# Optimization experiments

Measured on AMD Instinct MI355X. Metric: run time of the kernel, lower is better.

## Reference

```python
import jax, jax.numpy as jnp
import numpy as np
import math

B, S, D, H = 4, 512, 128, 4
HD = D // H
NEG = float(-2**32 + 1)

def _ln(x, g, b, eps=1e-8):
    m = jnp.mean(x, axis=-1, keepdims=True)
    v = jnp.var(x, axis=-1, keepdims=True)
    return (x - m) * jax.lax.rsqrt(v + eps) * g + b

def setup_inputs() -> dict:
    key = jax.random.key(0)
    ks = jax.random.split(key, 16)
    s = 0.02
    inp = {
        'embed': jax.random.normal(ks[0], (B, S, D), jnp.float32),
        'time_matrix_K': jax.random.normal(ks[1], (B, S, S, D), jnp.float32),
        'time_matrix_V': jax.random.normal(ks[2], (B, S, S, D), jnp.float32),
        # causal additive mask: large negative above diagonal (1--mask semantics)
        'attn_mask': jnp.where(jnp.triu(jnp.ones((S, S), bool), k=1), jnp.float32(-1e9), jnp.float32(0.0)),
        'padding_mask': jnp.zeros((B, S), bool),
        'wq': jax.random.normal(ks[3], (D, D), jnp.float32) * s,
        'bq': jnp.zeros((D,), jnp.float32),
        'wk': jax.random.normal(ks[4], (D, D), jnp.float32) * s,
        'bk': jnp.zeros((D,), jnp.float32),
        'wv': jax.random.normal(ks[5], (D, D), jnp.float32) * s,
        'bv': jnp.zeros((D,), jnp.float32),
        'wo': jax.random.normal(ks[6], (D, D), jnp.float32) * s,
        'bo': jnp.zeros((D,), jnp.float32),
        'ln1_g': jnp.ones((D,), jnp.float32),
        'ln1_b': jnp.zeros((D,), jnp.float32),
        'ln2_g': jnp.ones((D,), jnp.float32),
        'ln2_b': jnp.zeros((D,), jnp.float32),
        'w1': jax.random.normal(ks[7], (D, D), jnp.float32) * s,  # d_ff defaults to d_model
        'b1': jnp.zeros((D,), jnp.float32),
        'w2': jax.random.normal(ks[8], (D, D), jnp.float32) * s,
        'b2': jnp.zeros((D,), jnp.float32),
    }
    return inp

def reference(embed, time_matrix_K, time_matrix_V, attn_mask, padding_mask,
              wq, bq, wk, bk, wv, bv, wo, bo,
              ln1_g, ln1_b, ln2_g, ln2_b, w1, b1, w2, b2):
    # Pre-LN on Q only (K, V take raw embed), per original block
    Qn = _ln(embed, ln1_g, ln1_b)
    q = (Qn @ wq + bq).reshape(B, S, H, HD).transpose(0, 2, 1, 3)      # bhqd
    k = (embed @ wk + bk).reshape(B, S, H, HD).transpose(0, 2, 1, 3)   # bhkd
    v = (embed @ wv + bv).reshape(B, S, H, HD).transpose(0, 2, 1, 3)   # bhkd
    tmK = time_matrix_K.reshape(B, S, S, H, HD).transpose(0, 3, 1, 2, 4)  # bhqkd
    tmV = time_matrix_V.reshape(B, S, S, H, HD).transpose(0, 3, 1, 2, 4)  # bhqkd
    scale = math.sqrt(HD)
    energy = jnp.einsum('bhqd,bhkd->bhqk', q, k)
    energy = energy + jnp.einsum('bhqkd,bhqd->bhqk', tmK, q)
    energy = energy / scale
    energy = energy + attn_mask[None, None]
    energy = jnp.where(padding_mask[:, None, None, :], jnp.float32(NEG), energy)
    attn = jax.nn.softmax(energy, axis=-1)  # dropout is identity in eval
    O = jnp.einsum('bhqk,bhkd->bhqd', attn, v)
    O = O + jnp.einsum('bhqk,bhqkd->bhqd', attn, tmV)
    O = O.transpose(0, 2, 1, 3).reshape(B, S, D)
    O = O @ wo + bo
    x = Qn + O                      # residual adds LN'd Q, per original code
    x = _ln(x, ln2_g, ln2_b)
    ff = jax.nn.gelu(x @ w1 + b1, approximate=False) @ w2 + b2
    return ff + x
```

## Files before the change

kernel.cpp:

```cpp
#include <hip/hip_runtime.h>
#include <math.h>

#define Bsz 4
#define Ssz 512
#define Dsz 128
#define Hsz 4
#define HDsz 32
#define KT 64
#define NT 8

typedef float floatx4 __attribute__((ext_vector_type(4)));

static __device__ __forceinline__ float4 ldnt4(const float* p) {
    floatx4 v = __builtin_nontemporal_load(reinterpret_cast<const floatx4*>(p));
    float4 r; r.x = v.x; r.y = v.y; r.z = v.z; r.w = v.w;
    return r;
}

__global__ __launch_bounds__(128) void k_pre(
    const float* __restrict__ embed,
    const float* __restrict__ wq, const float* __restrict__ bq,
    const float* __restrict__ wk, const float* __restrict__ bk,
    const float* __restrict__ wv, const float* __restrict__ bv,
    const float* __restrict__ g1, const float* __restrict__ b1,
    float* __restrict__ Qn, float* __restrict__ Qs,
    float* __restrict__ Kp, float* __restrict__ Vp)
{
    __shared__ float xs[4][128];
    __shared__ float qs[4][128];
    const int t = threadIdx.x;
    const int row0 = blockIdx.x * 4;
    const int r = t >> 5;
    const int c = t & 31;
    const int d4 = c << 2;

    const float4* e4 = (const float4*)(embed + (size_t)row0 * Dsz);
    float4 x4 = e4[r * 32 + c];

    float s = x4.x + x4.y + x4.z + x4.w;
    #pragma unroll
    for (int o = 1; o < 32; o <<= 1) s += __shfl_xor(s, o);
    const float m = s * (1.0f / 128.0f);

    const float dx0 = x4.x - m, dx1 = x4.y - m, dx2 = x4.z - m, dx3 = x4.w - m;
    float vs = dx0*dx0 + dx1*dx1 + dx2*dx2 + dx3*dx3;
    #pragma unroll
    for (int o = 1; o < 32; o <<= 1) vs += __shfl_xor(vs, o);
    const float rstd = rsqrtf(vs * (1.0f / 128.0f) + 1e-8f);

    const float4 g4 = *(const float4*)(g1 + d4);
    const float4 bb4 = *(const float4*)(b1 + d4);
    float4 qn4;
    qn4.x = dx0 * rstd * g4.x + bb4.x;
    qn4.y = dx1 * rstd * g4.y + bb4.y;
    qn4.z = dx2 * rstd * g4.z + bb4.z;
    qn4.w = dx3 * rstd * g4.w + bb4.w;

    xs[r][d4+0] = x4.x; xs[r][d4+1] = x4.y; xs[r][d4+2] = x4.z; xs[r][d4+3] = x4.w;
    qs[r][d4+0] = qn4.x; qs[r][d4+1] = qn4.y; qs[r][d4+2] = qn4.z; qs[r][d4+3] = qn4.w;
    *(float4*)(Qn + (size_t)(row0 + r) * Dsz + d4) = qn4;
    __syncthreads();

    float aq[4] = {0,0,0,0}, ak[4] = {0,0,0,0}, av[4] = {0,0,0,0};
    for (int d = 0; d < 128; ++d) {
        const float wqv = wq[d*128 + t];
        const float wkv = wk[d*128 + t];
        const float wvv = wv[d*128 + t];
        #pragma unroll
        for (int rr = 0; rr < 4; ++rr) {
            aq[rr] += qs[rr][d] * wqv;
            ak[rr] += xs[rr][d] * wkv;
            av[rr] += xs[rr][d] * wvv;
        }
    }
    const float inv_scale = 0.17677669529663687f;
    const float bqv = bq[t], bkv = bk[t], bvv = bv[t];
    #pragma unroll
    for (int rr = 0; rr < 4; ++rr) {
        const size_t o = (size_t)(row0 + rr) * Dsz + t;
        Qs[o] = (aq[rr] + bqv) * inv_scale;
        Kp[o] = ak[rr] + bkv;
        Vp[o] = av[rr] + bvv;
    }
}

__global__ __launch_bounds__(256) void k_attn_tile(
    const float* __restrict__ tmK, const float* __restrict__ tmV,
    const float* __restrict__ Qs, const float* __restrict__ Kp,
    const float* __restrict__ Vp,
    float* __restrict__ Opart,
    float* __restrict__ ml)
{
    const int id = blockIdx.x;
    const int b = id & 3;
    const int q = (id >> 2) & (Ssz - 1);
    const int tile = id >> 11;
    const int k0 = tile * KT;
    if (k0 > q) return;

    const int t = threadIdx.x;
    const int w = t >> 6;
    const int lane = t & 63;
    const int rg = lane >> 3;
    const int fs = lane & 7;
    const int d4 = w * HDsz + fs * 4;

    const int nr_full = q - k0 + 1;
    const int nr = nr_full > KT ? KT : nr_full;
    const size_t rowq = (size_t)(b * Ssz + q);

    const float4 q4 = *(const float4*)(Qs + rowq * Dsz + d4);
    const float* tmKb = tmK + (rowq * (size_t)Ssz + k0) * Dsz;
    const float* Kb   = Kp + ((size_t)b * Ssz + k0) * Dsz;

    float p[8];
    #pragma unroll
    for (int i0 = 0; i0 < 8; i0 += 4) {
        float4 a[4], kv[4];
        #pragma unroll
        for (int u = 0; u < 4; ++u) {
            const int r = (i0 + u) * 8 + rg;
            if (r < nr) {
                a[u]  = ldnt4(tmKb + (size_t)r * Dsz + d4);
                kv[u] = *(const float4*)(Kb + (size_t)r * Dsz + d4);
            } else {
                a[u] = make_float4(0,0,0,0); kv[u] = make_float4(0,0,0,0);
            }
        }
        #pragma unroll
        for (int u = 0; u < 4; ++u) {
            const int r = (i0 + u) * 8 + rg;
            float val = q4.x*(a[u].x+kv[u].x) + q4.y*(a[u].y+kv[u].y)
                      + q4.z*(a[u].z+kv[u].z) + q4.w*(a[u].w+kv[u].w);
            val += __shfl_xor(val, 1);
            val += __shfl_xor(val, 2);
            val += __shfl_xor(val, 4);
            p[i0 + u] = (r < nr) ? val : -INFINITY;
        }
    }

    float mx = p[0];
    #pragma unroll
    for (int i = 1; i < 8; ++i) mx = fmaxf(mx, p[i]);
    mx = fmaxf(mx, __shfl_xor(mx, 8));
    mx = fmaxf(mx, __shfl_xor(mx, 16));
    mx = fmaxf(mx, __shfl_xor(mx, 32));

    float lsum = 0.0f;
    #pragma unroll
    for (int i = 0; i < 8; ++i) {
        p[i] = __expf(p[i] - mx);
        lsum += p[i];
    }
    lsum += __shfl_xor(lsum, 8);
    lsum += __shfl_xor(lsum, 16);
    lsum += __shfl_xor(lsum, 32);

    if (lane == 0) {
        float* mlp = ml + ((rowq * NT + tile) * Hsz + w) * 2;
        mlp[0] = mx;
        mlp[1] = lsum;
    }

    const float* tmVb = tmV + (rowq * (size_t)Ssz + k0) * Dsz;
    const float* Vb   = Vp + ((size_t)b * Ssz + k0) * Dsz;
    float4 acc = {0.0f, 0.0f, 0.0f, 0.0f};
    #pragma unroll
    for (int i0 = 0; i0 < 8; i0 += 4) {
        float4 a[4], vv[4];
        #pragma unroll
        for (int u = 0; u < 4; ++u) {
            const int r = (i0 + u) * 8 + rg;
            if (r < nr) {
                a[u]  = ldnt4(tmVb + (size_t)r * Dsz + d4);
                vv[u] = *(const float4*)(Vb + (size_t)r * Dsz + d4);
            } else {
                a[u] = make_float4(0,0,0,0); vv[u] = make_float4(0,0,0,0);
            }
        }
        #pragma unroll
        for (int u = 0; u < 4; ++u) {
            const float pw = p[i0 + u];
            acc.x += pw * (a[u].x + vv[u].x);
            acc.y += pw * (a[u].y + vv[u].y);
            acc.z += pw * (a[u].z + vv[u].z);
            acc.w += pw * (a[u].w + vv[u].w);
        }
    }
    #pragma unroll
    for (int o = 8; o < 64; o <<= 1) {
        acc.x += __shfl_xor(acc.x, o);
        acc.y += __shfl_xor(acc.y, o);
        acc.z += __shfl_xor(acc.z, o);
        acc.w += __shfl_xor(acc.w, o);
    }
    if (lane < 8) {
        float4* op = (float4*)(Opart + (rowq * NT + tile) * Dsz + d4);
        *op = acc;
    }
}

__global__ __launch_bounds__(128) void k_post(
    const float* __restrict__ Opart, const float* __restrict__ ml,
    const float* __restrict__ Qn,
    const float* __restrict__ wo, const float* __restrict__ bo,
    const float* __restrict__ g2, const float* __restrict__ b2ln,
    const float* __restrict__ w1, const float* __restrict__ b1,
    const float* __restrict__ w2, const float* __restrict__ b2,
    float* __restrict__ out)
{
    __shared__ float os[4][128];
    __shared__ float xn[4][128];
    __shared__ float hbuf[4][128];
    const int t = threadIdx.x;
    const int row0 = blockIdx.x * 4;
    const int r = t >> 5;
    const int c = t & 31;
    const int d4 = c << 2;
    const int h = t >> 5;

    #pragma unroll
    for (int rr = 0; rr < 4; ++rr) {
        const size_t rowq = (size_t)(row0 + rr);
        const int q = (int)(rowq & (Ssz - 1));
        const int nt = (q >> 6) + 1;
        float M = -INFINITY;
        for (int i = 0; i < nt; ++i)
            M = fmaxf(M, ml[((rowq * NT + i) * Hsz + h) * 2 + 0]);
        float den = 0.0f, o = 0.0f;
        for (int i = 0; i < nt; ++i) {
            const float* mlp = ml + ((rowq * NT + i) * Hsz + h) * 2;
            const float w = __expf(mlp[0] - M);
            den += w * mlp[1];
            o   += w * Opart[(rowq * NT + i) * Dsz + t];
        }
        os[rr][t] = o / den;
    }
    __syncthreads();

    float ao[4] = {0,0,0,0};
    for (int d = 0; d < 128; ++d) {
        const float wv = wo[d*128 + t];
        #pragma unroll
        for (int rr = 0; rr < 4; ++rr) ao[rr] += os[rr][d] * wv;
    }
    const float bov = bo[t];
    float xrow[4];
    #pragma unroll
    for (int rr = 0; rr < 4; ++rr)
        xrow[rr] = Qn[(size_t)(row0 + rr) * Dsz + t] + ao[rr] + bov;
    __syncthreads();
    #pragma unroll
    for (int rr = 0; rr < 4; ++rr) os[rr][t] = xrow[rr];
    __syncthreads();

    {
        const float4 x4 = *(const float4*)(&os[r][d4]);
        float s = x4.x + x4.y + x4.z + x4.w;
        #pragma unroll
        for (int o = 1; o < 32; o <<= 1) s += __shfl_xor(s, o);
        const float m = s * (1.0f / 128.0f);
        const float dx0 = x4.x - m, dx1 = x4.y - m, dx2 = x4.z - m, dx3 = x4.w - m;
        float vs = dx0*dx0 + dx1*dx1 + dx2*dx2 + dx3*dx3;
        #pragma unroll
        for (int o = 1; o < 32; o <<= 1) vs += __shfl_xor(vs, o);
        const float rstd = rsqrtf(vs * (1.0f / 128.0f) + 1e-8f);
        const float4 g4 = *(const float4*)(g2 + d4);
        const float4 bb4 = *(const float4*)(b2ln + d4);
        xn[r][d4+0] = dx0 * rstd * g4.x + bb4.x;
        xn[r][d4+1] = dx1 * rstd * g4.y + bb4.y;
        xn[r][d4+2] = dx2 * rstd * g4.z + bb4.z;
        xn[r][d4+3] = dx3 * rstd * g4.w + bb4.w;
    }
    __syncthreads();

    float a1[4] = {0,0,0,0};
    for (int d = 0; d < 128; ++d) {
        const float wv = w1[d*128 + t];
        #pragma unroll
        for (int rr = 0; rr < 4; ++rr) a1[rr] += xn[rr][d] * wv;
    }
    const float b1v = b1[t];
    #pragma unroll
    for (int rr = 0; rr < 4; ++rr) {
        const float hv = a1[rr] + b1v;
        hbuf[rr][t] = 0.5f * hv * (1.0f + erff(hv * 0.70710678118654752f));
    }
    __syncthreads();

    float a2[4] = {0,0,0,0};
    for (int d = 0; d < 128; ++d) {
        const float wv = w2[d*128 + t];
        #pragma unroll
        for (int rr = 0; rr < 4; ++rr) a2[rr] += hbuf[rr][d] * wv;
    }
    const float b2v = b2[t];
    #pragma unroll
    for (int rr = 0; rr < 4; ++rr)
        out[(size_t)(row0 + rr) * Dsz + t] = a2[rr] + b2v + xn[rr][t];
}

extern "C" void kernel_launch(void* const* d_in, const int* in_sizes, int n_in,
                              void* d_out, int out_size, void* d_ws, size_t ws_size,
                              hipStream_t stream) {
    const float* embed = (const float*)d_in[0];
    const float* tmK   = (const float*)d_in[1];
    const float* tmV   = (const float*)d_in[2];
    const float* wq = (const float*)d_in[5];
    const float* bq = (const float*)d_in[6];
    const float* wk = (const float*)d_in[7];
    const float* bk = (const float*)d_in[8];
    const float* wv = (const float*)d_in[9];
    const float* bv = (const float*)d_in[10];
    const float* wo = (const float*)d_in[11];
    const float* bo = (const float*)d_in[12];
    const float* g1 = (const float*)d_in[13];
    const float* b1l = (const float*)d_in[14];
    const float* g2 = (const float*)d_in[15];
    const float* b2l = (const float*)d_in[16];
    const float* w1 = (const float*)d_in[17];
    const float* b1 = (const float*)d_in[18];
    const float* w2 = (const float*)d_in[19];
    const float* b2 = (const float*)d_in[20];

    const size_t NE = (size_t)Bsz * Ssz * Dsz;
    float* ws = (float*)d_ws;
    float* Qn = ws;
    float* Qs = ws + NE;
    float* Kp = ws + 2 * NE;
    float* Vp = ws + 3 * NE;
    float* Opart = ws + 4 * NE;
    float* mlbuf = ws + 4 * NE + (size_t)Bsz * Ssz * NT * Dsz;

    k_pre<<<(Bsz * Ssz) / 4, 128, 0, stream>>>(embed, wq, bq, wk, bk, wv, bv,
                                               g1, b1l, Qn, Qs, Kp, Vp);
    k_attn_tile<<<Bsz * Ssz * NT, 256, 0, stream>>>(tmK, tmV, Qs, Kp, Vp,
                                                    Opart, mlbuf);
    k_post<<<(Bsz * Ssz) / 4, 128, 0, stream>>>(Opart, mlbuf, Qn, wo, bo,
                                                g2, b2l, w1, b1, w2, b2,
                                                (float*)d_out);
}
```

Measured before the change: 146.1 us.

## Precompute Q·K scores in a separate kernel instead of per-tile K loads

Adds a k_qk kernel that computes the full per-head Q·K^T score matrix into a workspace buffer. The attention tile kernel then loads only tmK rows and adds the precomputed score via a lane shuffle, which removes the repeated K-row loads in every tile. In exchange it adds a kernel launch and writes and reads a B*H*S*S float buffer, including the masked upper triangle. The workspace must be large enough to hold that buffer.

```diff
diff --git a/kernel.cpp b/kernel.cpp
--- a/kernel.cpp
+++ b/kernel.cpp
@@ -84,9 +84,51 @@
     }
 }
 
+__global__ __launch_bounds__(256) void k_qk(
+    const float* __restrict__ Qs, const float* __restrict__ Kp,
+    float* __restrict__ qk)
+{
+    __shared__ float Ql[64][32];
+    const int t = threadIdx.x;
+    const int id = blockIdx.x;
+    const int qb = id & 7;
+    const int h = (id >> 3) & 3;
+    const int b = id >> 5;
+
+    #pragma unroll
+    for (int i = 0; i < 2; ++i) {
+        const int idx = i * 256 + t;
+        const int row = idx >> 3;
+        const int j = idx & 7;
+        const float4 v = *(const float4*)(Qs + ((size_t)b * Ssz + qb*64 + row) * Dsz + h*HDsz + j*4);
+        *(float4*)(&Ql[row][j*4]) = v;
+    }
+    __syncthreads();
+
+    float4 kr0[8], kr1[8];
+    #pragma unroll
+    for (int j = 0; j < 8; ++j) {
+        kr0[j] = *(const float4*)(Kp + ((size_t)b * Ssz + t)       * Dsz + h*HDsz + j*4);
+        kr1[j] = *(const float4*)(Kp + ((size_t)b * Ssz + 256 + t) * Dsz + h*HDsz + j*4);
+    }
+
+    float* qkbase = qk + (((size_t)(b*Hsz + h)) * Ssz + (size_t)qb*64) * Ssz;
+    for (int ql = 0; ql < 64; ++ql) {
+        float a0 = 0.0f, a1 = 0.0f;
+        #pragma unroll
+        for (int j = 0; j < 8; ++j) {
+            const float4 qv = *(const float4*)(&Ql[ql][j*4]);
+            a0 += qv.x*kr0[j].x + qv.y*kr0[j].y + qv.z*kr0[j].z + qv.w*kr0[j].w;
+            a1 += qv.x*kr1[j].x + qv.y*kr1[j].y + qv.z*kr1[j].z + qv.w*kr1[j].w;
+        }
+        qkbase[(size_t)ql * Ssz + t]       = a0;
+        qkbase[(size_t)ql * Ssz + 256 + t] = a1;
+    }
+}
+
 __global__ __launch_bounds__(256) void k_attn_tile(
     const float* __restrict__ tmK, const float* __restrict__ tmV,
-    const float* __restrict__ Qs, const float* __restrict__ Kp,
+    const float* __restrict__ Qs, const float* __restrict__ qk,
     const float* __restrict__ Vp,
     float* __restrict__ Opart,
     float* __restrict__ ml)
@@ -111,31 +153,26 @@
 
     const float4 q4 = *(const float4*)(Qs + rowq * Dsz + d4);
     const float* tmKb = tmK + (rowq * (size_t)Ssz + k0) * Dsz;
-    const float* Kb   = Kp + ((size_t)b * Ssz + k0) * Dsz;
+    const float qkv = qk[((((size_t)(b*Hsz + w)) * Ssz + q) * Ssz) + k0 + lane];
 
     float p[8];
-    #pragma unroll
-    for (int i0 = 0; i0 < 8; i0 += 4) {
-        float4 a[4], kv[4];
-        #pragma unroll
-        for (int u = 0; u < 4; ++u) {
-            const int r = (i0 + u) * 8 + rg;
-            if (r < nr) {
-                a[u]  = ldnt4(tmKb + (size_t)r * Dsz + d4);
-                kv[u] = *(const float4*)(Kb + (size_t)r * Dsz + d4);
-            } else {
-                a[u] = make_float4(0,0,0,0); kv[u] = make_float4(0,0,0,0);
-            }
-        }
-        #pragma unroll
-        for (int u = 0; u < 4; ++u) {
-            const int r = (i0 + u) * 8 + rg;
-            float val = q4.x*(a[u].x+kv[u].x) + q4.y*(a[u].y+kv[u].y)
-                      + q4.z*(a[u].z+kv[u].z) + q4.w*(a[u].w+kv[u].w);
+    {
+        float4 a[8];
+        #pragma unroll
+        for (int u = 0; u < 8; ++u) {
+            const int r = u * 8 + rg;
+            a[u] = (r < nr) ? ldnt4(tmKb + (size_t)r * Dsz + d4)
+                            : make_float4(0,0,0,0);
+        }
+        #pragma unroll
+        for (int u = 0; u < 8; ++u) {
+            const int r = u * 8 + rg;
+            float val = q4.x*a[u].x + q4.y*a[u].y + q4.z*a[u].z + q4.w*a[u].w;
             val += __shfl_xor(val, 1);
             val += __shfl_xor(val, 2);
             val += __shfl_xor(val, 4);
-            p[i0 + u] = (r < nr) ? val : -INFINITY;
+            val += __shfl(qkv, u * 8 + rg);
+            p[u] = (r < nr) ? val : -INFINITY;
         }
     }
 
@@ -331,10 +368,12 @@
     float* Vp = ws + 3 * NE;
     float* Opart = ws + 4 * NE;
     float* mlbuf = ws + 4 * NE + (size_t)Bsz * Ssz * NT * Dsz;
+    float* qkbuf = mlbuf + (size_t)Bsz * Ssz * NT * Hsz * 2;
 
     k_pre<<<(Bsz * Ssz) / 4, 128, 0, stream>>>(embed, wq, bq, wk, bk, wv, bv,
                                                g1, b1l, Qn, Qs, Kp, Vp);
-    k_attn_tile<<<Bsz * Ssz * NT, 256, 0, stream>>>(tmK, tmV, Qs, Kp, Vp,
+    k_qk<<<Bsz * Hsz * (Ssz / 64), 256, 0, stream>>>(Qs, Kp, qkbuf);
+    k_attn_tile<<<Bsz * Ssz * NT, 256, 0, stream>>>(tmK, tmV, Qs, qkbuf, Vp,
                                                     Opart, mlbuf);
     k_post<<<(Bsz * Ssz) / 4, 128, 0, stream>>>(Opart, mlbuf, Qn, wo, bo,
                                                 g2, b2l, w1, b1, w2, b2,
```

Result: slower. 195.4 us (+33.8%).
